# Performance work log

Hardware: AMD Instinct MI355X
Metric: run time of the kernel (lower is better)

The kernel has to match this reference:

```python
import jax, jax.numpy as jnp
import numpy as np

NUM_HEADS = 32
HEAD_DIM = 128
ROPE_THETA = 10000.0


def _rope_tables(seq_len, head_dim, dtype):
    # inv freqs: 1 / theta^(2k/d), k = 0..d/2-1
    k = jnp.arange(head_dim // 2, dtype=jnp.float32)
    inv_freq = 1.0 / (ROPE_THETA ** (2.0 * k / head_dim))
    m = jnp.arange(seq_len, dtype=jnp.float32)
    freqs = jnp.outer(m, inv_freq)  # [S, D/2]
    return jnp.cos(freqs).astype(dtype), jnp.sin(freqs).astype(dtype)


def _apply_rope(x, cos, sin):
    # x: [B, H, S, D]; pairs are (x[2k], x[2k+1]) viewed as complex
    x0 = x[..., 0::2]
    x1 = x[..., 1::2]
    # broadcast cos/sin [S, D/2] -> [1, 1, S, D/2]
    out0 = x0 * cos - x1 * sin
    out1 = x0 * sin + x1 * cos
    # re-interleave
    return jnp.stack([out0, out1], axis=-1).reshape(x.shape)


def setup_inputs() -> dict:
    key = jax.random.key(0)
    k1, k2, k3 = jax.random.split(key, 3)
    B, S, D = 2, 2048, 4096
    x = jax.random.normal(k1, (B, S, D), dtype=jnp.float32)
    w_qkv = jax.random.normal(k2, (D, 3 * D), dtype=jnp.float32) * (D ** -0.5)
    w_proj = jax.random.normal(k3, (D, D), dtype=jnp.float32) * (D ** -0.5)
    b_proj = jnp.zeros((D,), dtype=jnp.float32)
    return {"x": x, "w_qkv": w_qkv, "w_proj": w_proj, "b_proj": b_proj}


def reference(x, w_qkv, w_proj, b_proj):
    B, S, D = x.shape
    H, Hd = NUM_HEADS, HEAD_DIM

    qkv = x @ w_qkv                                   # [B, S, 3D]
    qkv = qkv.reshape(B, S, 3, H, Hd)
    qkv = jnp.transpose(qkv, (2, 0, 3, 1, 4))          # [3, B, H, S, Hd]
    q, k, v = qkv[0], qkv[1], qkv[2]

    cos, sin = _rope_tables(S, Hd, x.dtype)
    q = _apply_rope(q, cos, sin)
    k = _apply_rope(k, cos, sin)

    scale = 1.0 / np.sqrt(Hd)
    scores = jnp.einsum('bhqd,bhkd->bhqk', q, k) * scale   # [B, H, S, S]
    causal = jnp.tril(jnp.ones((S, S), dtype=bool))
    scores = jnp.where(causal, scores, jnp.finfo(scores.dtype).min)
    attn = jax.nn.softmax(scores, axis=-1)
    out = jnp.einsum('bhqk,bhkd->bhqd', attn, v)            # [B, H, S, Hd]

    ctx = jnp.transpose(out, (0, 2, 1, 3)).reshape(B, S, H * Hd)
    return ctx @ w_proj + b_proj
```

## Files before the change

kernel.cpp:

```cpp
#include <hip/hip_runtime.h>
#include <stdint.h>

typedef unsigned short ushort_t;
typedef __attribute__((ext_vector_type(8))) short s16x8;
typedef __attribute__((ext_vector_type(4))) float f32x4;
typedef __attribute__((ext_vector_type(4))) unsigned short u16x4;

#define DEV __device__ __forceinline__

DEV ushort_t f2bf(float f) {
  union { float f; uint32_t u; } v; v.f = f;
  uint32_t r = (v.u + 0x7FFFu + ((v.u >> 16) & 1u)) >> 16;
  return (ushort_t)r;
}
DEV float bf2f(ushort_t u) {
  union { uint32_t u; float f; } v; v.u = ((uint32_t)u) << 16;
  return v.f;
}

DEV int swz(int row, int chunk) { return chunk ^ (row & 3) ^ ((row >> 2) & 3); }

#define GLD_LDS16(g, l)                                     \
  __builtin_amdgcn_global_load_lds(                         \
      (const __attribute__((address_space(1))) void*)(g),   \
      (__attribute__((address_space(3))) void*)(l), 16, 0, 0)

#define MFMA16(a, b, c) __builtin_amdgcn_mfma_f32_16x16x32_bf16((a), (b), (c), 0, 0, 0)

__global__ __launch_bounds__(256) void k_conv(const float* __restrict__ in,
                                              ushort_t* __restrict__ out, int n4) {
  int i = blockIdx.x * 256 + threadIdx.x;
  if (i >= n4) return;
  float4 v = ((const float4*)in)[i];
  u16x4 o;
  o[0] = f2bf(v.x); o[1] = f2bf(v.y); o[2] = f2bf(v.z); o[3] = f2bf(v.w);
  *((u16x4*)out + i) = o;
}

__global__ __launch_bounds__(256) void k_transpose_conv(const float* __restrict__ in,
                                                        ushort_t* __restrict__ out,
                                                        int R, int C) {
  __shared__ float tile[64][65];
  int c0 = blockIdx.x * 64, r0 = blockIdx.y * 64;
  int t = threadIdx.x;
#pragma unroll
  for (int i = 0; i < 4; ++i) {
    int e = (i * 256 + t) * 4;
    int rr = e >> 6, cc = e & 63;
    float4 v = *(const float4*)(in + (size_t)(r0 + rr) * C + (c0 + cc));
    tile[rr][cc] = v.x; tile[rr][cc + 1] = v.y;
    tile[rr][cc + 2] = v.z; tile[rr][cc + 3] = v.w;
  }
  __syncthreads();
#pragma unroll
  for (int i = 0; i < 4; ++i) {
    int e = (i * 256 + t) * 4;
    int cc = e >> 6, rr = e & 63;
    u16x4 o;
    o[0] = f2bf(tile[rr][cc]);     o[1] = f2bf(tile[rr + 1][cc]);
    o[2] = f2bf(tile[rr + 2][cc]); o[3] = f2bf(tile[rr + 3][cc]);
    *(u16x4*)(out + (size_t)(c0 + cc) * R + (r0 + rr)) = o;
  }
}

template <bool BF16OUT, bool ROPE>
__global__ __launch_bounds__(256, 3) void k_gemm_bt(const ushort_t* __restrict__ A,
                                                    const ushort_t* __restrict__ Bt,
                                                    ushort_t* __restrict__ Cb,
                                                    float* __restrict__ Cf,
                                                    const float* __restrict__ bias,
                                                    int M, int N, int K) {
  __shared__ ushort_t lA[128 * 32];
  __shared__ ushort_t lB[128 * 32];
  int t = threadIdx.x;
  int wv = t >> 6, lane = t & 63, quad = lane >> 4, lrow = lane & 15;
  int wr = wv >> 1, wc = wv & 1;
  int n0 = blockIdx.x * 128, m0 = blockIdx.y * 128;

  f32x4 acc[4][4];
#pragma unroll
  for (int i = 0; i < 4; ++i)
#pragma unroll
    for (int j = 0; j < 4; ++j) acc[i][j] = (f32x4){0.f, 0.f, 0.f, 0.f};

  for (int k0 = 0; k0 < K; k0 += 32) {
    __syncthreads();
#pragma unroll
    for (int c = 0; c < 2; ++c) {
      int se = (c * 256 + t) * 8;
      int row = se >> 5;
      int scn = (se >> 3) & 3;
      int col = swz(row, scn) * 8;
      GLD_LDS16(A + (size_t)(m0 + row) * K + k0 + col, lA + (c * 256 + wv * 64) * 8);
      GLD_LDS16(Bt + (size_t)(n0 + row) * K + k0 + col, lB + (c * 256 + wv * 64) * 8);
    }
    __syncthreads();
    s16x8 af[4], bfr[4];
#pragma unroll
    for (int i = 0; i < 4; ++i) {
      int row = wr * 64 + i * 16 + lrow;
      af[i] = *(const s16x8*)(lA + row * 32 + swz(row, quad) * 8);
    }
#pragma unroll
    for (int j = 0; j < 4; ++j) {
      int row = wc * 64 + j * 16 + lrow;
      bfr[j] = *(const s16x8*)(lB + row * 32 + swz(row, quad) * 8);
    }
#pragma unroll
    for (int i = 0; i < 4; ++i)
#pragma unroll
      for (int j = 0; j < 4; ++j) acc[i][j] = MFMA16(af[i], bfr[j], acc[i][j]);
  }

  bool do_rope = ROPE && (n0 < 8192);
  float sgn_sel = (lrow & 1) ? 1.f : -1.f;
#pragma unroll
  for (int j = 0; j < 4; ++j) {
    int gc = n0 + wc * 64 + j * 16 + lrow;
    float freq = 0.f;
    if (do_rope) {
      int p = (gc & 127) >> 1;
      freq = __expf(-(float)p * 0.14391156509165667f);
    }
#pragma unroll
    for (int i = 0; i < 4; ++i)
#pragma unroll
      for (int r = 0; r < 4; ++r) {
        int gr = m0 + wr * 64 + i * 16 + quad * 4 + r;
        float val = acc[i][j][r];
        if (do_rope) {
          float other = __shfl_xor(val, 1);
          float sv, cv;
          sincosf((float)(gr & 2047) * freq, &sv, &cv);
          val = fmaf(other, sgn_sel * sv, val * cv);
        }
        if (BF16OUT)
          Cb[(size_t)gr * N + gc] = f2bf(val);
        else
          Cf[(size_t)gr * N + gc] = val + bias[gc];
      }
  }
}

__global__ __launch_bounds__(256) void k_build_vt(const ushort_t* __restrict__ qkv,
                                                  ushort_t* __restrict__ vt) {
  const int S = 2048;
  int s0 = blockIdx.x * 64;
  int bh = blockIdx.y;
  int b = bh >> 5, h = bh & 31;
  __shared__ ushort_t tl[64][136];
  int t = threadIdx.x;
  const ushort_t* src = qkv + (size_t)(b * S + s0) * 12288 + 8192 + h * 128;
#pragma unroll
  for (int i = 0; i < 4; ++i) {
    int e = (i * 256 + t) * 8;
    int row = e >> 7, col = e & 127;
    *(s16x8*)&tl[row][col] = *(const s16x8*)(src + (size_t)row * 12288 + col);
  }
  __syncthreads();
  ushort_t* dst = vt + (size_t)bh * 128 * S;
#pragma unroll
  for (int i = 0; i < 4; ++i) {
    int e = (i * 256 + t) * 8;
    int d = e >> 6, ss = e & 63;
    s16x8 o;
#pragma unroll
    for (int j = 0; j < 8; ++j) o[j] = (short)tl[ss + j][d];
    *(s16x8*)(dst + (size_t)d * S + s0 + ss) = o;
  }
}

__global__ __launch_bounds__(256, 2) void k_attn(const ushort_t* __restrict__ qkv,
                                                 const ushort_t* __restrict__ vt,
                                                 ushort_t* __restrict__ ctx) {
  const int S = 2048;
  int qt = blockIdx.x, bh = blockIdx.y;
  int b = bh >> 5, h = bh & 31;
  int q0 = qt * 128;
  int t = threadIdx.x;
  int wv = t >> 6, lane = t & 63, quad = lane >> 4, lrow = lane & 15;

  __shared__ ushort_t lK[64 * 128];
  __shared__ ushort_t lV[128 * 64];
  __shared__ ushort_t lP[4][32][72];

  const ushort_t* qp = qkv + (size_t)(b * S) * 12288 + h * 128;
  const ushort_t* kp = qp + 4096;
  const ushort_t* vp = vt + (size_t)bh * 128 * S;

  s16x8 qf[2][4];
  int qrb = q0 + wv * 32;
#pragma unroll
  for (int ti = 0; ti < 2; ++ti)
#pragma unroll
    for (int ks = 0; ks < 4; ++ks)
      qf[ti][ks] = *(const s16x8*)(qp + (size_t)(qrb + ti * 16 + lrow) * 12288 +
                                   ks * 32 + quad * 8);

  f32x4 O[2][8];
#pragma unroll
  for (int ti = 0; ti < 2; ++ti)
#pragma unroll
    for (int f = 0; f < 8; ++f) O[ti][f] = (f32x4){0.f, 0.f, 0.f, 0.f};
  float m_i[2][4], l_i[2][4];
#pragma unroll
  for (int ti = 0; ti < 2; ++ti)
#pragma unroll
    for (int r = 0; r < 4; ++r) { m_i[ti][r] = -__builtin_inff(); l_i[ti][r] = 0.f; }

  const float scale = 0.08838834764831845f;
  int qhi = q0 + 127;

  for (int kv0 = 0; kv0 <= qhi; kv0 += 64) {
    __syncthreads();
    {
      int ck = lane & 15;
      int cv = lane & 7;
#pragma unroll
      for (int it = 0; it < 4; ++it) {
        int slot = wv * 4 + it;
        int rowk = slot * 4 + (lane >> 4);
        int cpk = (ck & 8) | ((ck & 7) ^ (rowk & 7));
        GLD_LDS16(kp + (size_t)(kv0 + rowk) * 12288 + cpk * 8, lK + slot * 512);
        int rowv = slot * 8 + (lane >> 3);
        int cpv = cv ^ (rowv & 7);
        GLD_LDS16(vp + (size_t)rowv * S + kv0 + cpv * 8, lV + slot * 512);
      }
    }
    __syncthreads();

    f32x4 sc[2][4];
#pragma unroll
    for (int ti = 0; ti < 2; ++ti)
#pragma unroll
      for (int nt = 0; nt < 4; ++nt) sc[ti][nt] = (f32x4){0.f, 0.f, 0.f, 0.f};
#pragma unroll
    for (int ks = 0; ks < 4; ++ks) {
      s16x8 bk[4];
#pragma unroll
      for (int nt = 0; nt < 4; ++nt) {
        int row = nt * 16 + lrow;
        int cc = ks * 4 + quad;
        int cp = (cc & 8) | ((cc & 7) ^ (row & 7));
        bk[nt] = *(const s16x8*)(lK + row * 128 + cp * 8);
      }
#pragma unroll
      for (int ti = 0; ti < 2; ++ti)
#pragma unroll
        for (int nt = 0; nt < 4; ++nt) sc[ti][nt] = MFMA16(qf[ti][ks], bk[nt], sc[ti][nt]);
    }

#pragma unroll
    for (int ti = 0; ti < 2; ++ti) {
      int qr = qrb + ti * 16 + quad * 4;
      float mt[4];
#pragma unroll
      for (int r = 0; r < 4; ++r) mt[r] = -__builtin_inff();
      float pvl[4][4];
#pragma unroll
      for (int nt = 0; nt < 4; ++nt) {
        int kc = kv0 + nt * 16 + lrow;
#pragma unroll
        for (int r = 0; r < 4; ++r) {
          float sv = sc[ti][nt][r] * scale;
          if (kc > qr + r) sv = -__builtin_inff();
          pvl[nt][r] = sv;
          mt[r] = fmaxf(mt[r], sv);
        }
      }
#pragma unroll
      for (int r = 0; r < 4; ++r)
#pragma unroll
        for (int off = 1; off < 16; off <<= 1)
          mt[r] = fmaxf(mt[r], __shfl_xor(mt[r], off, 16));

      float al[4], ls[4];
#pragma unroll
      for (int r = 0; r < 4; ++r) {
        float mn = fmaxf(m_i[ti][r], mt[r]);
        al[r] = __expf(m_i[ti][r] - mn);
        m_i[ti][r] = mn;
        ls[r] = 0.f;
      }
#pragma unroll
      for (int nt = 0; nt < 4; ++nt)
#pragma unroll
        for (int r = 0; r < 4; ++r) {
          float p = __expf(pvl[nt][r] - m_i[ti][r]);
          ushort_t pu = f2bf(p);
          lP[wv][ti * 16 + quad * 4 + r][nt * 16 + lrow] = pu;
          ls[r] += bf2f(pu);
        }
#pragma unroll
      for (int r = 0; r < 4; ++r) {
#pragma unroll
        for (int off = 1; off < 16; off <<= 1) ls[r] += __shfl_xor(ls[r], off, 16);
        l_i[ti][r] = al[r] * l_i[ti][r] + ls[r];
      }
#pragma unroll
      for (int f = 0; f < 8; ++f)
#pragma unroll
        for (int r = 0; r < 4; ++r) O[ti][f][r] *= al[r];
    }

#pragma unroll
    for (int ks = 0; ks < 2; ++ks) {
      s16x8 pa[2];
#pragma unroll
      for (int ti = 0; ti < 2; ++ti)
        pa[ti] = *(const s16x8*)&lP[wv][ti * 16 + lrow][ks * 32 + quad * 8];
#pragma unroll
      for (int f = 0; f < 8; ++f) {
        int row = f * 16 + lrow;
        int cc = ks * 4 + quad;
        int cp = cc ^ (row & 7);
        s16x8 bv = *(const s16x8*)(lV + row * 64 + cp * 8);
#pragma unroll
        for (int ti = 0; ti < 2; ++ti) O[ti][f] = MFMA16(pa[ti], bv, O[ti][f]);
      }
    }
  }

#pragma unroll
  for (int ti = 0; ti < 2; ++ti) {
    float inv[4];
#pragma unroll
    for (int r = 0; r < 4; ++r) inv[r] = 1.f / l_i[ti][r];
#pragma unroll
    for (int f = 0; f < 8; ++f)
#pragma unroll
      for (int r = 0; r < 4; ++r) {
        size_t idx = (size_t)(b * S + qrb + ti * 16 + quad * 4 + r) * 4096 +
                     h * 128 + f * 16 + lrow;
        ctx[idx] = f2bf(O[ti][f][r] * inv[r]);
      }
  }
}

extern "C" void kernel_launch(void* const* d_in, const int* in_sizes, int n_in,
                              void* d_out, int out_size, void* d_ws, size_t ws_size,
                              hipStream_t stream) {
  const float* x      = (const float*)d_in[0];
  const float* w_qkv  = (const float*)d_in[1];
  const float* w_proj = (const float*)d_in[2];
  const float* b_proj = (const float*)d_in[3];
  float* out = (float*)d_out;

  char* ws = (char*)d_ws;
  ushort_t* xb     = (ushort_t*)(ws);
  ushort_t* wqkvt  = (ushort_t*)(ws + 33554432ULL);
  ushort_t* wprojt = (ushort_t*)(ws + 134217728ULL);
  ushort_t* qkvb   = (ushort_t*)(ws + 167772160ULL);
  ushort_t* vt     = (ushort_t*)(ws + 268435456ULL);
  ushort_t* ctx    = (ushort_t*)(ws + 301989888ULL);

  k_conv<<<16384, 256, 0, stream>>>(x, xb, 16777216 / 4);
  k_transpose_conv<<<dim3(192, 64), 256, 0, stream>>>(w_qkv, wqkvt, 4096, 12288);
  k_transpose_conv<<<dim3(64, 64), 256, 0, stream>>>(w_proj, wprojt, 4096, 4096);
  k_gemm_bt<true, true><<<dim3(96, 32), 256, 0, stream>>>(xb, wqkvt, qkvb, nullptr,
                                                          nullptr, 4096, 12288, 4096);
  k_build_vt<<<dim3(32, 64), 256, 0, stream>>>(qkvb, vt);
  k_attn<<<dim3(16, 64), 256, 0, stream>>>(qkvb, vt, ctx);
  k_gemm_bt<false, false><<<dim3(32, 32), 256, 0, stream>>>(ctx, wprojt, nullptr, out,
                                                            b_proj, 4096, 4096, 4096);
}
```

Measured before the change: 1.380 ms.

## Rewrite GEMM with 256x256 tiles, 4-stage LDS pipeline and XCD-aware block remap

```diff
diff --git a/kernel.cpp b/kernel.cpp
--- a/kernel.cpp
+++ b/kernel.cpp
@@ -17,8 +17,6 @@
   union { uint32_t u; float f; } v; v.u = ((uint32_t)u) << 16;
   return v.f;
 }
-
-DEV int swz(int row, int chunk) { return chunk ^ (row & 3) ^ ((row >> 2) & 3); }
 
 #define GLD_LDS16(g, l)                                     \
   __builtin_amdgcn_global_load_lds(                         \
@@ -64,53 +62,102 @@
 }
 
 template <bool BF16OUT, bool ROPE>
-__global__ __launch_bounds__(256, 3) void k_gemm_bt(const ushort_t* __restrict__ A,
+__global__ __launch_bounds__(512, 2) void k_gemm_bt(const ushort_t* __restrict__ A,
                                                     const ushort_t* __restrict__ Bt,
                                                     ushort_t* __restrict__ Cb,
                                                     float* __restrict__ Cf,
                                                     const float* __restrict__ bias,
                                                     int M, int N, int K) {
-  __shared__ ushort_t lA[128 * 32];
-  __shared__ ushort_t lB[128 * 32];
+  __shared__ __align__(16) ushort_t lA[4 * 256 * 32];
+  __shared__ __align__(16) ushort_t lB[4 * 256 * 32];
   int t = threadIdx.x;
   int wv = t >> 6, lane = t & 63, quad = lane >> 4, lrow = lane & 15;
-  int wr = wv >> 1, wc = wv & 1;
-  int n0 = blockIdx.x * 128, m0 = blockIdx.y * 128;
-
-  f32x4 acc[4][4];
-#pragma unroll
-  for (int i = 0; i < 4; ++i)
+  int wr = wv >> 2, wc = wv & 3;
+
+  int nbx = gridDim.x;
+  int nwg = nbx * gridDim.y;
+  int id = blockIdx.y * nbx + blockIdx.x;
+  int qq = nwg >> 3;
+  int sw = (id & 7) * qq + (id >> 3);
+  int n0 = (sw % nbx) * 256;
+  int m0 = (sw / nbx) * 256;
+
+  int srow = t >> 2;
+  int gch = (t & 3) ^ ((t >> 3) & 3);
+  const ushort_t* gA0 = A + (size_t)(m0 + srow) * K + gch * 8;
+  const ushort_t* gA1 = gA0 + (size_t)128 * K;
+  const ushort_t* gB0 = Bt + (size_t)(n0 + srow) * K + gch * 8;
+  const ushort_t* gB1 = gB0 + (size_t)128 * K;
+  int ldst = wv * 512;
+
+  int xorv = (lrow >> 1) & 3;
+  int aoff = (wr * 128 + lrow) * 32 + ((quad ^ xorv) * 8);
+  int boff = (wc * 64 + lrow) * 32 + ((quad ^ xorv) * 8);
+
+  f32x4 acc[8][4];
+#pragma unroll
+  for (int i = 0; i < 8; ++i)
 #pragma unroll
     for (int j = 0; j < 4; ++j) acc[i][j] = (f32x4){0.f, 0.f, 0.f, 0.f};
 
-  for (int k0 = 0; k0 < K; k0 += 32) {
-    __syncthreads();
-#pragma unroll
-    for (int c = 0; c < 2; ++c) {
-      int se = (c * 256 + t) * 8;
-      int row = se >> 5;
-      int scn = (se >> 3) & 3;
-      int col = swz(row, scn) * 8;
-      GLD_LDS16(A + (size_t)(m0 + row) * K + k0 + col, lA + (c * 256 + wv * 64) * 8);
-      GLD_LDS16(Bt + (size_t)(n0 + row) * K + k0 + col, lB + (c * 256 + wv * 64) * 8);
-    }
-    __syncthreads();
-    s16x8 af[4], bfr[4];
-#pragma unroll
-    for (int i = 0; i < 4; ++i) {
-      int row = wr * 64 + i * 16 + lrow;
-      af[i] = *(const s16x8*)(lA + row * 32 + swz(row, quad) * 8);
-    }
-#pragma unroll
-    for (int j = 0; j < 4; ++j) {
-      int row = wc * 64 + j * 16 + lrow;
-      bfr[j] = *(const s16x8*)(lB + row * 32 + swz(row, quad) * 8);
-    }
-#pragma unroll
-    for (int i = 0; i < 4; ++i)
-#pragma unroll
-      for (int j = 0; j < 4; ++j) acc[i][j] = MFMA16(af[i], bfr[j], acc[i][j]);
-  }
+  int nt = K >> 5;
+
+  auto stageA = [&](int tt) {
+    int buf = tt & 3;
+    size_t ko = (size_t)tt * 32;
+    ushort_t* la = lA + buf * 8192 + ldst;
+    GLD_LDS16(gA0 + ko, la);
+    GLD_LDS16(gA1 + ko, la + 4096);
+  };
+  auto stageB = [&](int tt) {
+    int buf = tt & 3;
+    size_t ko = (size_t)tt * 32;
+    ushort_t* lb = lB + buf * 8192 + ldst;
+    GLD_LDS16(gB0 + ko, lb);
+    GLD_LDS16(gB1 + ko, lb + 4096);
+  };
+
+  stageA(0); stageB(0);
+  stageA(1); stageB(1);
+  stageA(2); stageB(2);
+
+#define TILE_BODY(BUFV, DOSTAGE, TT)                                     \
+  {                                                                      \
+    const ushort_t* ba = lA + (BUFV) * 8192;                             \
+    const ushort_t* bb = lB + (BUFV) * 8192;                             \
+    s16x8 af[4], bfr[4];                                                 \
+    _Pragma("unroll") for (int j = 0; j < 4; ++j)                        \
+        bfr[j] = *(const s16x8*)(bb + boff + j * 512);                   \
+    _Pragma("unroll") for (int i = 0; i < 4; ++i)                        \
+        af[i] = *(const s16x8*)(ba + aoff + i * 512);                    \
+    if (DOSTAGE) stageA((TT) + 3);                                       \
+    __builtin_amdgcn_s_setprio(1);                                       \
+    _Pragma("unroll") for (int i = 0; i < 4; ++i)                        \
+      _Pragma("unroll") for (int j = 0; j < 4; ++j)                      \
+          acc[i][j] = MFMA16(af[i], bfr[j], acc[i][j]);                  \
+    __builtin_amdgcn_s_setprio(0);                                       \
+    _Pragma("unroll") for (int i = 0; i < 4; ++i)                        \
+        af[i] = *(const s16x8*)(ba + aoff + (i + 4) * 512);              \
+    if (DOSTAGE) stageB((TT) + 3);                                       \
+    __builtin_amdgcn_s_setprio(1);                                       \
+    _Pragma("unroll") for (int i = 0; i < 4; ++i)                        \
+      _Pragma("unroll") for (int j = 0; j < 4; ++j)                      \
+          acc[i + 4][j] = MFMA16(af[i], bfr[j], acc[i + 4][j]);          \
+    __builtin_amdgcn_s_setprio(0);                                       \
+  }
+
+  for (int tt = 0; tt < nt - 2; ++tt) {
+    asm volatile("s_waitcnt vmcnt(8)" ::: "memory");
+    __builtin_amdgcn_s_barrier();
+    TILE_BODY(tt & 3, (tt < nt - 3), tt);
+  }
+  asm volatile("s_waitcnt vmcnt(4)" ::: "memory");
+  __builtin_amdgcn_s_barrier();
+  TILE_BODY((nt - 2) & 3, false, nt - 2);
+  asm volatile("s_waitcnt vmcnt(0)" ::: "memory");
+  __builtin_amdgcn_s_barrier();
+  TILE_BODY((nt - 1) & 3, false, nt - 1);
+#undef TILE_BODY
 
   bool do_rope = ROPE && (n0 < 8192);
   float sgn_sel = (lrow & 1) ? 1.f : -1.f;
@@ -123,10 +170,10 @@
       freq = __expf(-(float)p * 0.14391156509165667f);
     }
 #pragma unroll
-    for (int i = 0; i < 4; ++i)
+    for (int i = 0; i < 8; ++i)
 #pragma unroll
       for (int r = 0; r < 4; ++r) {
-        int gr = m0 + wr * 64 + i * 16 + quad * 4 + r;
+        int gr = m0 + wr * 128 + i * 16 + quad * 4 + r;
         float val = acc[i][j][r];
         if (do_rope) {
           float other = __shfl_xor(val, 1);
@@ -357,10 +404,10 @@
   k_conv<<<16384, 256, 0, stream>>>(x, xb, 16777216 / 4);
   k_transpose_conv<<<dim3(192, 64), 256, 0, stream>>>(w_qkv, wqkvt, 4096, 12288);
   k_transpose_conv<<<dim3(64, 64), 256, 0, stream>>>(w_proj, wprojt, 4096, 4096);
-  k_gemm_bt<true, true><<<dim3(96, 32), 256, 0, stream>>>(xb, wqkvt, qkvb, nullptr,
+  k_gemm_bt<true, true><<<dim3(48, 16), 512, 0, stream>>>(xb, wqkvt, qkvb, nullptr,
                                                           nullptr, 4096, 12288, 4096);
   k_build_vt<<<dim3(32, 64), 256, 0, stream>>>(qkvb, vt);
   k_attn<<<dim3(16, 64), 256, 0, stream>>>(qkvb, vt, ctx);
-  k_gemm_bt<false, false><<<dim3(32, 32), 256, 0, stream>>>(ctx, wprojt, nullptr, out,
+  k_gemm_bt<false, false><<<dim3(16, 16), 512, 0, stream>>>(ctx, wprojt, nullptr, out,
                                                             b_proj, 4096, 4096, 4096);
 }
```

After: 1.356 ms. About the same (-1.8%).
